# Performance work log

Measured on AMD Instinct MI355X. Metric: run time of the kernel, lower is better.

## Reference

```python
import jax, jax.numpy as jnp
import numpy as np

CIN = 256
WINDOWS = (2, 4, 6)
LN_EPS = 1e-5


def _conv1x1(x, w, b):
    # x: (N,C,H,W), w: (O,C), b: (O,)
    return jnp.einsum('nchw,oc->nohw', x, w) + b[None, :, None, None]


def _pos_encoding(C, H, W):
    # Faithful to SinCosPositionalEncoding2D (incl. its w-major flatten + raw view)
    gw, gh = jnp.meshgrid(jnp.arange(W, dtype=jnp.float32),
                          jnp.arange(H, dtype=jnp.float32), indexing='ij')
    pd = C // 4
    omega = 1.0 / (10000.0 ** (jnp.arange(pd, dtype=jnp.float32) / pd))
    ow = gw.reshape(-1)[:, None] * omega[None, :]
    oh = gh.reshape(-1)[:, None] * omega[None, :]
    pe = jnp.concatenate([jnp.sin(ow), jnp.cos(ow), jnp.sin(oh), jnp.cos(oh)], axis=1)  # (W*H, C)
    return pe.reshape(1, C, H, W)  # raw row-major reinterpret, matching torch .view


def _unfold(x, kh, kw, sh, sw):
    # torch F.unfold semantics: (N,C,H,W) -> (N, C*kh*kw, L), L row-major over (oh, ow)
    N, C, H, W = x.shape
    oh = (H - kh) // sh + 1
    ow = (W - kw) // sw + 1
    ih = (jnp.arange(oh) * sh)[:, None] + jnp.arange(kh)[None, :]  # (oh,kh)
    iw = (jnp.arange(ow) * sw)[:, None] + jnp.arange(kw)[None, :]  # (ow,kw)
    p = x[:, :, ih[:, None, :, None], iw[None, :, None, :]]       # (N,C,oh,ow,kh,kw)
    return jnp.transpose(p, (0, 1, 4, 5, 2, 3)).reshape(N, C * kh * kw, oh * ow)


def _fold(p, H, W, kh, kw, sh, sw):
    # torch F.fold semantics: overlap-add scatter back to (N,C,H,W)
    N = p.shape[0]
    C = p.shape[1] // (kh * kw)
    oh = (H - kh) // sh + 1
    ow = (W - kw) // sw + 1
    p = jnp.transpose(p.reshape(N, C, kh, kw, oh, ow), (0, 1, 4, 5, 2, 3))  # (N,C,oh,ow,kh,kw)
    ih = (jnp.arange(oh) * sh)[:, None] + jnp.arange(kh)[None, :]
    iw = (jnp.arange(ow) * sw)[:, None] + jnp.arange(kw)[None, :]
    out = jnp.zeros((N, C, H, W), p.dtype)
    return out.at[:, :, ih[:, None, :, None], iw[None, :, None, :]].add(p)


def _psa(x, ch_wv_w, ch_wv_b, ch_wq_w, ch_wq_b, ch_wz_w, ch_wz_b, ln_g, ln_b,
         sp_wv_w, sp_wv_b, sp_wq_w, sp_wq_b):
    # Polarized Self-Attention (parallel), input (N,C,H',W')
    N, C, Hh, Ww = x.shape
    C2 = C // 2
    HW = Hh * Ww
    # channel-only branch
    wv = _conv1x1(x, ch_wv_w, ch_wv_b).reshape(N, C2, HW)
    wq = jax.nn.softmax(_conv1x1(x, ch_wq_w, ch_wq_b).reshape(N, HW), axis=-1)
    z = jnp.einsum('ncl,nl->nc', wv, wq)                       # (N, C2)
    wz = jnp.einsum('nc,oc->no', z, ch_wz_w) + ch_wz_b         # (N, C)
    m = wz.mean(-1, keepdims=True)
    v = ((wz - m) ** 2).mean(-1, keepdims=True)
    ch_w = jax.nn.sigmoid((wz - m) / jnp.sqrt(v + LN_EPS) * ln_g + ln_b)
    out_ch = x * ch_w[:, :, None, None]
    # spatial-only branch
    sv = _conv1x1(x, sp_wv_w, sp_wv_b).reshape(N, C2, HW)
    sq = jax.nn.softmax(_conv1x1(x, sp_wq_w, sp_wq_b).mean(axis=(2, 3)), axis=-1)  # (N,C2)
    sp_w = jax.nn.sigmoid(jnp.einsum('nc,ncl->nl', sq, sv)).reshape(N, 1, Hh, Ww)
    return out_ch + x * sp_w


def _forward(x, w_exp, b_exp, w_res, b_res, w_fus, b_fus,
             ch_wv_w, ch_wv_b, ch_wq_w, ch_wq_b, ch_wz_w, ch_wz_b, ln_g, ln_b,
             sp_wv_w, sp_wv_b, sp_wq_w, sp_wq_b):
    N, C, H, W = x.shape
    expx = _conv1x1(x, w_exp, b_exp)                 # (N, 3C, H, W)
    branches = jnp.split(expx, len(WINDOWS), axis=1)
    pos = _pos_encoding(C, H, W)
    outs = []
    for i, win in enumerate(WINDOWS):
        sh, sw = H // win, W // win
        kh, kw = sh + H % win, sw + W % win
        K = kh * kw
        u = _unfold(branches[i], kh, kw, sh, sw).reshape(N, C, win * win, K)
        pu = _unfold(pos, kh, kw, sh, sw).reshape(1, C, win * win, K)
        a = _psa(u + pu, ch_wv_w, ch_wv_b, ch_wq_w, ch_wq_b, ch_wz_w, ch_wz_b,
                 ln_g, ln_b, sp_wv_w, sp_wv_b, sp_wq_w, sp_wq_b)
        a = a.reshape(N, C * K, win * win)           # raw view, matching torch
        cnt = _fold(jnp.ones_like(a), H, W, kh, kw, sh, sw)
        f = _fold(a, H, W, kh, kw, sh, sw) / cnt
        outs.append(f)
    out = _conv1x1(jnp.concatenate(outs, axis=1) + expx, w_res, b_res) + x
    return _conv1x1(out, w_fus, b_fus)


def setup_inputs() -> dict:
    key = jax.random.key(0)
    ks = jax.random.split(key, 10)
    C, C2 = CIN, CIN // 2
    s = 0.02
    nrm = lambda k, shp: jax.random.normal(k, shp, jnp.float32) * s
    return {
        'x': jax.random.normal(ks[0], (8, C, 64, 64), jnp.float32),
        'w_exp': nrm(ks[1], (3 * C, C)), 'b_exp': jnp.zeros((3 * C,), jnp.float32),
        'w_res': nrm(ks[2], (C, 3 * C)), 'b_res': jnp.zeros((C,), jnp.float32),
        'w_fus': nrm(ks[3], (C, C)), 'b_fus': jnp.zeros((C,), jnp.float32),
        'ch_wv_w': nrm(ks[4], (C2, C)), 'ch_wv_b': jnp.zeros((C2,), jnp.float32),
        'ch_wq_w': nrm(ks[5], (1, C)), 'ch_wq_b': jnp.zeros((1,), jnp.float32),
        'ch_wz_w': nrm(ks[6], (C, C2)), 'ch_wz_b': jnp.zeros((C,), jnp.float32),
        'ln_g': jnp.ones((C,), jnp.float32), 'ln_b': jnp.zeros((C,), jnp.float32),
        'sp_wv_w': nrm(ks[7], (C2, C)), 'sp_wv_b': jnp.zeros((C2,), jnp.float32),
        'sp_wq_w': nrm(ks[8], (C2, C)), 'sp_wq_b': jnp.zeros((C2,), jnp.float32),
    }


def reference(x, w_exp, b_exp, w_res, b_res, w_fus, b_fus,
              ch_wv_w, ch_wv_b, ch_wq_w, ch_wq_b, ch_wz_w, ch_wz_b, ln_g, ln_b,
              sp_wv_w, sp_wv_b, sp_wq_w, sp_wq_b):
    return _forward(x, w_exp, b_exp, w_res, b_res, w_fus, b_fus,
                    ch_wv_w, ch_wv_b, ch_wq_w, ch_wq_b, ch_wz_w, ch_wz_b, ln_g, ln_b,
                    sp_wv_w, sp_wv_b, sp_wq_w, sp_wq_b)
```

## Files before the change

### kernel.cpp

```cpp
#include <hip/hip_runtime.h>
#include <cstddef>


#define HW 4096
typedef unsigned short ushort_t;
typedef __attribute__((ext_vector_type(8))) short bf16x8;
typedef __attribute__((ext_vector_type(4))) float floatx4;

__device__ __forceinline__ ushort_t f2bf(float f) {
    unsigned u = __float_as_uint(f);
    u += 0x7FFF + ((u >> 16) & 1);
    return (ushort_t)(u >> 16);
}

__device__ __forceinline__ int cnt1f(int y, int sh, int kh, int win) {
    int t = y - kh + sh;
    int lo = t > 0 ? t / sh : 0;
    int hi = min(win - 1, y / sh);
    return hi - lo + 1;
}

__device__ __forceinline__ float posval(int f) {
    int row = f >> 8, col = f & 255;
    int a = row >> 6, b = row & 63;
    int g = col >> 6, k = col & 63;
    float omega = expf(-(float)k * (9.2103403719761836f / 64.f));
    float arg = (g < 2 ? (float)a : (float)b) * omega;
    return (g & 1) ? cosf(arg) : sinf(arg);
}

__global__ __launch_bounds__(256) void pos_both(
    float* __restrict__ pos, float* __restrict__ posT)
{
    int idx = blockIdx.x * 256 + threadIdx.x;
    pos[idx] = posval(idx);
    int p = idx >> 8, c = idx & 255;
    posT[idx] = posval(c * 4096 + p);
}

__global__ __launch_bounds__(256) void zero_kernel(float* __restrict__ p, int n) {
    int i = blockIdx.x * 256 + threadIdx.x;
    if (i < n) p[i] = 0.f;
}

__global__ __launch_bounds__(256) void trans_x(
    const float* __restrict__ x, ushort_t* __restrict__ xbT)
{
    __shared__ float L[32][37];
    int n = blockIdx.z;
    int p0 = blockIdx.x * 32, c0 = blockIdx.y * 32;
    int t = threadIdx.x;
    int cc = t >> 3, p4 = (t & 7) * 4;
    const float* src = x + (((size_t)(n * 256 + c0 + cc)) << 12) + p0 + p4;
    float4 v = *(const float4*)src;
    L[cc][p4] = v.x; L[cc][p4 + 1] = v.y; L[cc][p4 + 2] = v.z; L[cc][p4 + 3] = v.w;
    __syncthreads();
    int pp = t >> 3, c4 = (t & 7) * 4;
    unsigned lo = (unsigned)f2bf(L[c4][pp]) | ((unsigned)f2bf(L[c4 + 1][pp]) << 16);
    unsigned hi = (unsigned)f2bf(L[c4 + 2][pp]) | ((unsigned)f2bf(L[c4 + 3][pp]) << 16);
    *(uint2*)&xbT[(((size_t)(n << 12)) + p0 + pp) * 256 + c0 + c4] = make_uint2(lo, hi);
}

__global__ __launch_bounds__(256) void conv_bf16(
    const float* __restrict__ src, ushort_t* __restrict__ dst, int nelem)
{
    int i = blockIdx.x * 256 + threadIdx.x;
    if (i < nelem) dst[i] = f2bf(src[i]);
}

__global__ __launch_bounds__(256) void prep_g(
    const float* __restrict__ W_exp, const float* __restrict__ b_exp,
    const float* __restrict__ wq, const float* __restrict__ wq_b,
    float* __restrict__ g, float* __restrict__ c0out)
{
    int i = blockIdx.x, ks = blockIdx.y, tid = threadIdx.x;
    __shared__ float wql[32];
    __shared__ float red[256];
    if (tid < 32) wql[tid] = wq[ks * 32 + tid];
    __syncthreads();
    const float* Wb = W_exp + ((size_t)(i * 256 + ks * 32)) * 256 + tid;
    float acc = 0.f;
    #pragma unroll 8
    for (int j = 0; j < 32; ++j) acc = fmaf(wql[j], Wb[(size_t)j * 256], acc);
    atomicAdd(&g[i * 256 + tid], acc);
    red[tid] = (tid < 32) ? wql[tid] * b_exp[i * 256 + ks * 32 + tid] : 0.f;
    __syncthreads();
    for (int s = 128; s > 0; s >>= 1) { if (tid < s) red[tid] += red[tid + s]; __syncthreads(); }
    if (tid == 0) atomicAdd(&c0out[i], red[0] + (ks == 0 ? wq_b[0] : 0.f));
}

__global__ __launch_bounds__(256) void prep_wcomb(
    const float* __restrict__ W_fus, const float* __restrict__ W_res,
    const float* __restrict__ b_res, const float* __restrict__ b_fus,
    ushort_t* __restrict__ Wcat, float* __restrict__ biasc)
{
    int o = blockIdx.x, jb = blockIdx.y, tid = threadIdx.x;
    __shared__ float wrow[256];
    __shared__ float red[256];
    wrow[tid] = W_fus[o * 256 + tid];
    __syncthreads();
    int j = jb * 256 + tid;
    float acc = 0.f;
    #pragma unroll 8
    for (int c = 0; c < 256; ++c) acc = fmaf(wrow[c], W_res[(size_t)c * 768 + j], acc);
    Wcat[o * 1024 + 256 + j] = f2bf(acc);
    if (jb == 0) {
        Wcat[o * 1024 + tid] = f2bf(wrow[tid]);
        red[tid] = wrow[tid] * b_res[tid];
        __syncthreads();
        for (int s = 128; s > 0; s >>= 1) { if (tid < s) red[tid] += red[tid + s]; __syncthreads(); }
        if (tid == 0) biasc[o] = red[0] + b_fus[o];
    }
}

__global__ __launch_bounds__(256) void xbar_kernel(
    const float* __restrict__ x, const float* __restrict__ pos,
    float* __restrict__ xbar_all, float* __restrict__ xbar6,
    float* __restrict__ posbar, float* __restrict__ posbar6)
{
    int c = blockIdx.x, n = blockIdx.y, tid = threadIdx.x;
    const float* src = (n < 8) ? x + (((size_t)(n * 256 + c)) << 12)
                               : pos + (((size_t)c) << 12);
    float sa = 0.f, s6 = 0.f;
    #pragma unroll
    for (int k = 0; k < 4; ++k) {
        int f4 = tid + k * 256;
        float4 v = *(const float4*)(src + f4 * 4);
        int p = f4 * 4;
        int y = p >> 6, xx = p & 63;
        float cy = (float)cnt1f(y, 10, 14, 6);
        float c0_ = cy * (float)cnt1f(xx + 0, 10, 14, 6);
        float c1_ = cy * (float)cnt1f(xx + 1, 10, 14, 6);
        float c2_ = cy * (float)cnt1f(xx + 2, 10, 14, 6);
        float c3_ = cy * (float)cnt1f(xx + 3, 10, 14, 6);
        sa += v.x + v.y + v.z + v.w;
        s6 += c0_ * v.x + c1_ * v.y + c2_ * v.z + c3_ * v.w;
    }
    __shared__ float red[256];
    red[tid] = sa; __syncthreads();
    for (int s = 128; s > 0; s >>= 1) { if (tid < s) red[tid] += red[tid + s]; __syncthreads(); }
    float ra = red[0]; __syncthreads();
    red[tid] = s6; __syncthreads();
    for (int s = 128; s > 0; s >>= 1) { if (tid < s) red[tid] += red[tid + s]; __syncthreads(); }
    float r6 = red[0];
    if (tid == 0) {
        if (n < 8) { xbar_all[n * 256 + c] = ra; xbar6[n * 256 + c] = r6; }
        else       { posbar[c] = ra;             posbar6[c] = r6; }
    }
}

__global__ __launch_bounds__(512) void qdot_kernel(
    const float* __restrict__ x, const float* __restrict__ pos,
    const float* __restrict__ g, const float* __restrict__ c0in,
    const float* __restrict__ wq, float* __restrict__ qdot)
{
    int n = blockIdx.y, tid = threadIdx.x;
    int ph = tid & 127, cq = tid >> 7;
    int p = blockIdx.x * 128 + ph;
    __shared__ float gl[768];
    __shared__ float wql[256];
    __shared__ float4 red4[512];
    for (int k = tid; k < 768; k += 512) gl[k] = g[k];
    if (tid < 256) wql[tid] = wq[tid];
    __syncthreads();
    const float* xp = x + (((size_t)n) << 20) + p;
    const float* pp = pos + p;
    float q0 = 0.f, q1 = 0.f, q2 = 0.f, qp = 0.f;
    #pragma unroll 4
    for (int c = cq * 64; c < cq * 64 + 64; ++c) {
        float xv = xp[(size_t)c << 12];
        float pv = pp[(size_t)c << 12];
        q0 = fmaf(gl[c], xv, q0);
        q1 = fmaf(gl[256 + c], xv, q1);
        q2 = fmaf(gl[512 + c], xv, q2);
        qp = fmaf(wql[c], pv, qp);
    }
    red4[tid] = make_float4(q0, q1, q2, qp);
    __syncthreads();
    if (tid < 128) {
        float4 a = red4[tid], b = red4[128 + tid], cc = red4[256 + tid], d = red4[384 + tid];
        float rp = a.w + b.w + cc.w + d.w;
        qdot[((0 * 8 + n) << 12) + p] = a.x + b.x + cc.x + d.x + rp + c0in[0];
        qdot[((1 * 8 + n) << 12) + p] = a.y + b.y + cc.y + d.y + rp + c0in[1];
        qdot[((2 * 8 + n) << 12) + p] = a.z + b.z + cc.z + d.z + rp + c0in[2];
    }
}

__global__ __launch_bounds__(256) void ubar_split(
    const float* __restrict__ W_exp, const float* __restrict__ b_exp,
    const float* __restrict__ xbar_all, const float* __restrict__ xbar6,
    const float* __restrict__ posbar, const float* __restrict__ posbar6,
    float* __restrict__ ubar)
{
    int i = blockIdx.x, n = blockIdx.y, ks = blockIdx.z, tid = threadIdx.x;
    int b = i * 8 + n;
    __shared__ float xbl[32];
    const float* xsrc = ((i < 2) ? xbar_all : xbar6) + n * 256 + ks * 32;
    if (tid < 32) xbl[tid] = xsrc[tid];
    __syncthreads();
    const float* Wr = W_exp + ((size_t)(i * 256 + tid)) * 256 + ks * 32;
    float acc = 0.f;
    #pragma unroll 8
    for (int j = 0; j < 32; ++j) acc = fmaf(Wr[j], xbl[j], acc);
    if (ks == 0) {
        int win = 2 * (i + 1), sh = 64 / win, kh = sh + 64 % win;
        float Li = (float)(win * win * kh * kh);
        acc += b_exp[i * 256 + tid] * Li + ((i < 2) ? posbar : posbar6)[tid];
    }
    atomicAdd(&ubar[b * 256 + tid], acc);
}

__global__ __launch_bounds__(256) void pass_b_h(
    const float* __restrict__ qdot, const float* __restrict__ ubar_raw,
    const float* __restrict__ sp_wq_w, const float* __restrict__ sp_wq_b,
    const float* __restrict__ sp_wv_w, const float* __restrict__ sp_wv_b,
    const float* __restrict__ W_exp, const float* __restrict__ b_exp,
    float* __restrict__ Mn, float* __restrict__ invZn,
    float* __restrict__ w_eff, float* __restrict__ h, float* __restrict__ btot)
{
    int i = blockIdx.x, n = blockIdx.y, tid = threadIdx.x;
    int b = i * 8 + n;
    int win = 2 * (i + 1), sh = 64 / win, kh = sh + 64 % win;
    float invL = 1.f / (float)(win * win * kh * kh);
    const float* qd = qdot + (((size_t)b) << 12);
    __shared__ float red[256];
    __shared__ float ub[256];
    __shared__ float spq[128];
    __shared__ float we[256];
    float m = -1e30f;
    for (int p = tid; p < HW; p += 256) m = fmaxf(m, qd[p]);
    red[tid] = m; __syncthreads();
    for (int s = 128; s > 0; s >>= 1) { if (tid < s) red[tid] = fmaxf(red[tid], red[tid + s]); __syncthreads(); }
    float M = red[0]; __syncthreads();
    float z = 0.f;
    for (int p = tid; p < HW; p += 256) {
        int y = p >> 6, xx = p & 63;
        float cf = (float)(cnt1f(y, sh, kh, win) * cnt1f(xx, sh, kh, win));
        z += cf * expf(qd[p] - M);
    }
    red[tid] = z; __syncthreads();
    for (int s = 128; s > 0; s >>= 1) { if (tid < s) red[tid] += red[tid + s]; __syncthreads(); }
    float Z = red[0]; __syncthreads();
    if (tid == 0) { Mn[b] = M; invZn[b] = 1.f / Z; }
    ub[tid] = ubar_raw[b * 256 + tid] * invL;
    __syncthreads();
    float sl = -1e30f;
    if (tid < 128) {
        float a = sp_wq_b[tid];
        #pragma unroll 8
        for (int c = 0; c < 256; ++c) a = fmaf(sp_wq_w[tid * 256 + c], ub[c], a);
        sl = a;
    }
    red[tid] = sl; __syncthreads();
    for (int s = 128; s > 0; s >>= 1) { if (tid < s) red[tid] = fmaxf(red[tid], red[tid + s]); __syncthreads(); }
    float m2 = red[0]; __syncthreads();
    float e = (tid < 128) ? expf(sl - m2) : 0.f;
    red[tid] = e; __syncthreads();
    for (int s = 128; s > 0; s >>= 1) { if (tid < s) red[tid] += red[tid + s]; __syncthreads(); }
    float S2 = red[0]; __syncthreads();
    if (tid < 128) spq[tid] = e / S2;
    __syncthreads();
    float a = 0.f;
    #pragma unroll 8
    for (int c2 = 0; c2 < 128; ++c2) a = fmaf(spq[c2], sp_wv_w[c2 * 256 + tid], a);
    w_eff[b * 256 + tid] = a;
    we[tid] = a;
    red[tid] = (tid < 128) ? spq[tid] * sp_wv_b[tid] : 0.f;
    __syncthreads();
    for (int s = 128; s > 0; s >>= 1) { if (tid < s) red[tid] += red[tid + s]; __syncthreads(); }
    float beff = red[0]; __syncthreads();
    const float* Wb = W_exp + (size_t)i * 65536 + tid;
    float hacc = 0.f;
    #pragma unroll 8
    for (int oc = 0; oc < 256; ++oc) hacc = fmaf(we[oc], Wb[(size_t)oc * 256], hacc);
    h[b * 256 + tid] = hacc;
    red[tid] = we[tid] * b_exp[i * 256 + tid];
    __syncthreads();
    for (int s = 128; s > 0; s >>= 1) { if (tid < s) red[tid] += red[tid + s]; __syncthreads(); }
    if (tid == 0) btot[b] = red[0] + beff;
}

__global__ __launch_bounds__(512) void spw_t_kernel(
    const float* __restrict__ x, const float* __restrict__ pos,
    const float* __restrict__ h, const float* __restrict__ weff,
    const float* __restrict__ qdot, const float* __restrict__ Mn,
    const float* __restrict__ invZn, const float* __restrict__ btot,
    float* __restrict__ spw, float* __restrict__ tbuf)
{
    int n = blockIdx.y, tid = threadIdx.x;
    int ph = tid & 127, cq = tid >> 7;
    int p = blockIdx.x * 128 + ph;
    __shared__ float hl[768], wl[768];
    __shared__ float4 red4[512];
    for (int k = tid; k < 768; k += 512) {
        int i = k >> 8, c = k & 255;
        hl[k] = h[(i * 8 + n) * 256 + c];
        wl[k] = weff[(i * 8 + n) * 256 + c];
    }
    __syncthreads();
    const float* xp = x + (((size_t)n) << 20) + p;
    const float* pp = pos + p;
    float a0 = 0.f, a1 = 0.f, a2 = 0.f;
    #pragma unroll 4
    for (int c = cq * 64; c < cq * 64 + 64; ++c) {
        float xv = xp[(size_t)c << 12];
        float pv = pp[(size_t)c << 12];
        a0 += hl[c] * xv + wl[c] * pv;
        a1 += hl[256 + c] * xv + wl[256 + c] * pv;
        a2 += hl[512 + c] * xv + wl[512 + c] * pv;
    }
    red4[tid] = make_float4(a0, a1, a2, 0.f);
    __syncthreads();
    if (tid < 128) {
        float4 aa = red4[tid], bb = red4[128 + tid], cc = red4[256 + tid], dd = red4[384 + tid];
        float av[3] = {aa.x + bb.x + cc.x + dd.x,
                       aa.y + bb.y + cc.y + dd.y,
                       aa.z + bb.z + cc.z + dd.z};
        int y = p >> 6, xx = p & 63;
        #pragma unroll
        for (int i = 0; i < 3; ++i) {
            int b = i * 8 + n;
            int win = 2 * (i + 1), sh = 64 / win, kh = sh + 64 % win;
            float cf = (float)(cnt1f(y, sh, kh, win) * cnt1f(xx, sh, kh, win));
            int idx = (b << 12) + p;
            spw[idx] = 1.f / (1.f + expf(-(av[i] + btot[b])));
            tbuf[idx] = cf * expf(qdot[idx] - Mn[b]) * invZn[b];
        }
    }
}

__global__ __launch_bounds__(256) void xq_kernel(
    const float* __restrict__ x, const float* __restrict__ pos,
    const float* __restrict__ tbuf, float* __restrict__ xq, float* __restrict__ posq)
{
    int c = blockIdx.x, n = blockIdx.y, tid = threadIdx.x;
    const float* xr = x + (((size_t)(n * 256 + c)) << 12);
    const float* pr = pos + (((size_t)c) << 12);
    float ax[3] = {0.f, 0.f, 0.f}, ap[3] = {0.f, 0.f, 0.f};
    #pragma unroll
    for (int k = 0; k < 4; ++k) {
        int f4 = tid + k * 256;
        float4 xv = *(const float4*)(xr + f4 * 4);
        float4 pv = *(const float4*)(pr + f4 * 4);
        #pragma unroll
        for (int i = 0; i < 3; ++i) {
            float4 tv = *(const float4*)(tbuf + (((size_t)(i * 8 + n)) << 12) + f4 * 4);
            ax[i] += tv.x * xv.x + tv.y * xv.y + tv.z * xv.z + tv.w * xv.w;
            ap[i] += tv.x * pv.x + tv.y * pv.y + tv.z * pv.z + tv.w * pv.w;
        }
    }
    __shared__ float red[256];
    #pragma unroll
    for (int i = 0; i < 3; ++i) {
        red[tid] = ax[i]; __syncthreads();
        for (int s = 128; s > 0; s >>= 1) { if (tid < s) red[tid] += red[tid + s]; __syncthreads(); }
        float rx = red[0]; __syncthreads();
        red[tid] = ap[i]; __syncthreads();
        for (int s = 128; s > 0; s >>= 1) { if (tid < s) red[tid] += red[tid + s]; __syncthreads(); }
        float rp = red[0]; __syncthreads();
        if (tid == 0) { xq[(i * 8 + n) * 256 + c] = rx; posq[(i * 8 + n) * 256 + c] = rp; }
    }
}

__global__ __launch_bounds__(256) void pass_d_uq(
    const float* __restrict__ W_exp, const float* __restrict__ b_exp,
    const float* __restrict__ xq, const float* __restrict__ posq,
    const float* __restrict__ ch_wv_w, const float* __restrict__ ch_wv_b,
    const float* __restrict__ ch_wz_w, const float* __restrict__ ch_wz_b,
    const float* __restrict__ ln_g, const float* __restrict__ ln_b,
    float* __restrict__ ch_w)
{
    int i = blockIdx.x, n = blockIdx.y, tid = threadIdx.x;
    int b = i * 8 + n;
    __shared__ float xql[256];
    __shared__ float uql[256];
    __shared__ float zz[128];
    __shared__ float red[256];
    xql[tid] = xq[b * 256 + tid];
    __syncthreads();
    float acc = b_exp[i * 256 + tid] + posq[b * 256 + tid];
    const float* Wr = W_exp + ((size_t)(i * 256 + tid)) * 256;
    #pragma unroll 8
    for (int cin = 0; cin < 256; ++cin) acc = fmaf(Wr[cin], xql[cin], acc);
    uql[tid] = acc;
    __syncthreads();
    if (tid < 128) {
        float a = ch_wv_b[tid];
        #pragma unroll 8
        for (int c = 0; c < 256; ++c) a = fmaf(ch_wv_w[tid * 256 + c], uql[c], a);
        zz[tid] = a;
    }
    __syncthreads();
    float wz = ch_wz_b[tid];
    #pragma unroll 8
    for (int c2 = 0; c2 < 128; ++c2) wz = fmaf(ch_wz_w[tid * 128 + c2], zz[c2], wz);
    red[tid] = wz; __syncthreads();
    for (int s = 128; s > 0; s >>= 1) { if (tid < s) red[tid] += red[tid + s]; __syncthreads(); }
    float mean = red[0] * (1.f / 256.f); __syncthreads();
    float d = wz - mean;
    red[tid] = d * d; __syncthreads();
    for (int s = 128; s > 0; s >>= 1) { if (tid < s) red[tid] += red[tid + s]; __syncthreads(); }
    float var = red[0] * (1.f / 256.f);
    float xn = d / sqrtf(var + 1e-5f);
    ch_w[b * 256 + tid] = 1.f / (1.f + expf(-(xn * ln_g[tid] + ln_b[tid])));
}

__global__ __launch_bounds__(256) void gemm_expT(
    const ushort_t* __restrict__ Wb, const ushort_t* __restrict__ XT,
    const float* __restrict__ bias, const float* __restrict__ posT,
    const float* __restrict__ chw, const float* __restrict__ spw,
    ushort_t* __restrict__ OutT)
{
    __shared__ ushort_t As[128 * 40];
    __shared__ ushort_t Bs[128 * 40];
    int n = blockIdx.z;
    int p0 = blockIdx.x * 128;
    int o0 = blockIdx.y * 128;
    int t = threadIdx.x;
    int lane = t & 63, wave = t >> 6;
    int wm = (wave & 1) * 64, wn = (wave >> 1) * 64;
    int lr = lane & 15, lk = (lane >> 4) * 8;
    int ar = t >> 2, ac = (t & 3) * 8;
    const ushort_t* A0 = Wb + (size_t)(o0 + ar) * 256 + ac;
    const ushort_t* A1 = Wb + (size_t)(o0 + ar + 64) * 256 + ac;
    const ushort_t* B0 = XT + (((size_t)(n << 12)) + p0 + ar) * 256 + ac;
    const ushort_t* B1 = XT + (((size_t)(n << 12)) + p0 + ar + 64) * 256 + ac;
    floatx4 acc[4][4] = {};
    for (int k0 = 0; k0 < 256; k0 += 32) {
        uint4 a0 = *(const uint4*)(A0 + k0);
        uint4 a1 = *(const uint4*)(A1 + k0);
        uint4 b0 = *(const uint4*)(B0 + k0);
        uint4 b1 = *(const uint4*)(B1 + k0);
        __syncthreads();
        *(uint4*)&As[ar * 40 + ac] = a0;
        *(uint4*)&As[(ar + 64) * 40 + ac] = a1;
        *(uint4*)&Bs[ar * 40 + ac] = b0;
        *(uint4*)&Bs[(ar + 64) * 40 + ac] = b1;
        __syncthreads();
        bf16x8 af[4], bfr[4];
        #pragma unroll
        for (int mi = 0; mi < 4; ++mi)
            af[mi] = *(const bf16x8*)&As[(wm + mi * 16 + lr) * 40 + lk];
        #pragma unroll
        for (int ni = 0; ni < 4; ++ni)
            bfr[ni] = *(const bf16x8*)&Bs[(wn + ni * 16 + lr) * 40 + lk];
        #pragma unroll
        for (int mi = 0; mi < 4; ++mi)
            #pragma unroll
            for (int ni = 0; ni < 4; ++ni)
                acc[mi][ni] = __builtin_amdgcn_mfma_f32_16x16x32_bf16(
                    af[mi], bfr[ni], acc[mi][ni], 0, 0, 0);
    }
    int col = lane & 15, rb = (lane >> 4) * 4;
    int ibr = o0 >> 8;
    int bi = ibr * 8 + n;
    float sv[4]; int pv_[4];
    #pragma unroll
    for (int ni = 0; ni < 4; ++ni) {
        int p = p0 + wn + ni * 16 + col;
        pv_[ni] = p;
        sv[ni] = spw[(bi << 12) + p];
    }
    #pragma unroll
    for (int mi = 0; mi < 4; ++mi) {
        int o = o0 + wm + mi * 16 + rb;
        int c = o & 255;
        float4 bo = *(const float4*)&bias[o];
        float4 cw = *(const float4*)&chw[bi * 256 + c];
        #pragma unroll
        for (int ni = 0; ni < 4; ++ni) {
            int p = pv_[ni];
            float4 q = *(const float4*)&posT[p * 256 + c];
            floatx4 v = acc[mi][ni];
            float s = sv[ni];
            float e0 = v[0] + bo.x, e1 = v[1] + bo.y, e2 = v[2] + bo.z, e3 = v[3] + bo.w;
            float r0 = e0 + (e0 + q.x) * (cw.x + s);
            float r1 = e1 + (e1 + q.y) * (cw.y + s);
            float r2 = e2 + (e2 + q.z) * (cw.z + s);
            float r3 = e3 + (e3 + q.w) * (cw.w + s);
            unsigned lo = (unsigned)f2bf(r0) | ((unsigned)f2bf(r1) << 16);
            unsigned hi = (unsigned)f2bf(r2) | ((unsigned)f2bf(r3) << 16);
            *(uint2*)&OutT[(((size_t)(n << 12)) + p) * 768 + o] = make_uint2(lo, hi);
        }
    }
}

__global__ __launch_bounds__(256) void gemm_out(
    const ushort_t* __restrict__ Wcat, const ushort_t* __restrict__ XT,
    const ushort_t* __restrict__ CT, const float* __restrict__ biasc,
    float* __restrict__ Out)
{
    __shared__ ushort_t As[128 * 40];
    __shared__ ushort_t Bs[128 * 40];
    int n = blockIdx.z;
    int p0 = blockIdx.x * 128;
    int o0 = blockIdx.y * 128;
    int t = threadIdx.x;
    int lane = t & 63, wave = t >> 6;
    int wm = (wave & 1) * 64, wn = (wave >> 1) * 64;
    int lr = lane & 15, lk = (lane >> 4) * 8;
    int ar = t >> 2, ac = (t & 3) * 8;
    const ushort_t* A0 = Wcat + (size_t)(o0 + ar) * 1024 + ac;
    const ushort_t* A1 = Wcat + (size_t)(o0 + ar + 64) * 1024 + ac;
    const ushort_t* BX0 = XT + (((size_t)(n << 12)) + p0 + ar) * 256 + ac;
    const ushort_t* BX1 = XT + (((size_t)(n << 12)) + p0 + ar + 64) * 256 + ac;
    const ushort_t* BC0 = CT + (((size_t)(n << 12)) + p0 + ar) * 768 + ac;
    const ushort_t* BC1 = CT + (((size_t)(n << 12)) + p0 + ar + 64) * 768 + ac;
    floatx4 acc[4][4] = {};
    for (int k0 = 0; k0 < 1024; k0 += 32) {
        const ushort_t* pb0 = (k0 < 256) ? (BX0 + k0) : (BC0 + (k0 - 256));
        const ushort_t* pb1 = (k0 < 256) ? (BX1 + k0) : (BC1 + (k0 - 256));
        uint4 a0 = *(const uint4*)(A0 + k0);
        uint4 a1 = *(const uint4*)(A1 + k0);
        uint4 b0 = *(const uint4*)pb0;
        uint4 b1 = *(const uint4*)pb1;
        __syncthreads();
        *(uint4*)&As[ar * 40 + ac] = a0;
        *(uint4*)&As[(ar + 64) * 40 + ac] = a1;
        *(uint4*)&Bs[ar * 40 + ac] = b0;
        *(uint4*)&Bs[(ar + 64) * 40 + ac] = b1;
        __syncthreads();
        bf16x8 af[4], bfr[4];
        #pragma unroll
        for (int mi = 0; mi < 4; ++mi)
            af[mi] = *(const bf16x8*)&As[(wm + mi * 16 + lr) * 40 + lk];
        #pragma unroll
        for (int ni = 0; ni < 4; ++ni)
            bfr[ni] = *(const bf16x8*)&Bs[(wn + ni * 16 + lr) * 40 + lk];
        #pragma unroll
        for (int mi = 0; mi < 4; ++mi)
            #pragma unroll
            for (int ni = 0; ni < 4; ++ni)
                acc[mi][ni] = __builtin_amdgcn_mfma_f32_16x16x32_bf16(
                    af[mi], bfr[ni], acc[mi][ni], 0, 0, 0);
    }
    int col = lane & 15, rb = (lane >> 4) * 4;
    #pragma unroll
    for (int mi = 0; mi < 4; ++mi) {
        int o = o0 + wm + mi * 16 + rb;
        float4 bo = *(const float4*)&biasc[o];
        #pragma unroll
        for (int r = 0; r < 4; ++r) {
            float br = (r == 0) ? bo.x : (r == 1) ? bo.y : (r == 2) ? bo.z : bo.w;
            #pragma unroll
            for (int ni = 0; ni < 4; ++ni) {
                int p = p0 + wn + ni * 16 + col;
                Out[(((size_t)(n * 256 + o + r)) << 12) + p] = acc[mi][ni][r] + br;
            }
        }
    }
}

extern "C" void kernel_launch(void* const* d_in, const int* in_sizes, int n_in,
                              void* d_out, int out_size, void* d_ws, size_t ws_size,
                              hipStream_t stream) {
    const float* x        = (const float*)d_in[0];
    const float* w_exp    = (const float*)d_in[1];
    const float* b_exp    = (const float*)d_in[2];
    const float* w_res    = (const float*)d_in[3];
    const float* b_res    = (const float*)d_in[4];
    const float* w_fus    = (const float*)d_in[5];
    const float* b_fus    = (const float*)d_in[6];
    const float* ch_wv_w  = (const float*)d_in[7];
    const float* ch_wv_b  = (const float*)d_in[8];
    const float* ch_wq_w  = (const float*)d_in[9];
    const float* ch_wq_b  = (const float*)d_in[10];
    const float* ch_wz_w  = (const float*)d_in[11];
    const float* ch_wz_b  = (const float*)d_in[12];
    const float* ln_g     = (const float*)d_in[13];
    const float* ln_b     = (const float*)d_in[14];
    const float* sp_wv_w  = (const float*)d_in[15];
    const float* sp_wv_b  = (const float*)d_in[16];
    const float* sp_wq_w  = (const float*)d_in[17];
    const float* sp_wq_b  = (const float*)d_in[18];
    float* out = (float*)d_out;
    float* ws  = (float*)d_ws;

    float*    pos   = ws + 0;
    float*    posT  = ws + 1048576;
    ushort_t* xbT   = (ushort_t*)(ws + 2097152);
    ushort_t* exT   = (ushort_t*)(ws + 6291456);
    ushort_t* wexpb = (ushort_t*)(ws + 18874368);
    ushort_t* Wcat  = (ushort_t*)(ws + 18972672);
    float*    qdot  = ws + 19103744;
    float*    tbuf  = ws + 19202048;
    float*    spw   = ws + 19300352;
    float*    g     = ws + 19398656;
    float*    c0v   = ws + 19399424;
    float*    ubar  = ws + 19399428;
    float*    xba   = ws + 19405572;
    float*    xb6   = ws + 19407620;
    float*    pba   = ws + 19409668;
    float*    pb6   = ws + 19409924;
    float*    Mn    = ws + 19410180;
    float*    iZ    = ws + 19410204;
    float*    weff  = ws + 19410228;
    float*    btot  = ws + 19416372;
    float*    hb    = ws + 19416396;
    float*    xq    = ws + 19422540;
    float*    posq  = ws + 19428684;
    float*    chw   = ws + 19434828;
    float*    biasc = ws + 19440972;

    pos_both<<<4096, 256, 0, stream>>>(pos, posT);
    zero_kernel<<<28, 256, 0, stream>>>(g, 6916);
    trans_x<<<dim3(128, 8, 8), 256, 0, stream>>>(x, xbT);
    conv_bf16<<<768, 256, 0, stream>>>(w_exp, wexpb, 196608);
    prep_g<<<dim3(3, 8), 256, 0, stream>>>(w_exp, b_exp, ch_wq_w, ch_wq_b, g, c0v);
    prep_wcomb<<<dim3(256, 3), 256, 0, stream>>>(w_fus, w_res, b_res, b_fus, Wcat, biasc);

    xbar_kernel<<<dim3(256, 9), 256, 0, stream>>>(x, pos, xba, xb6, pba, pb6);
    qdot_kernel<<<dim3(32, 8), 512, 0, stream>>>(x, pos, g, c0v, ch_wq_w, qdot);
    ubar_split<<<dim3(3, 8, 8), 256, 0, stream>>>(w_exp, b_exp, xba, xb6, pba, pb6, ubar);
    pass_b_h<<<dim3(3, 8), 256, 0, stream>>>(qdot, ubar, sp_wq_w, sp_wq_b,
                                             sp_wv_w, sp_wv_b, w_exp, b_exp,
                                             Mn, iZ, weff, hb, btot);
    spw_t_kernel<<<dim3(32, 8), 512, 0, stream>>>(x, pos, hb, weff, qdot, Mn, iZ,
                                                  btot, spw, tbuf);
    xq_kernel<<<dim3(256, 8), 256, 0, stream>>>(x, pos, tbuf, xq, posq);
    pass_d_uq<<<dim3(3, 8), 256, 0, stream>>>(w_exp, b_exp, xq, posq,
                                              ch_wv_w, ch_wv_b, ch_wz_w, ch_wz_b,
                                              ln_g, ln_b, chw);

    gemm_expT<<<dim3(32, 6, 8), 256, 0, stream>>>(wexpb, xbT, b_exp, posT, chw, spw, exT);
    gemm_out<<<dim3(32, 2, 8), 256, 0, stream>>>(Wcat, xbT, exT, biasc, out);
}
```

Baseline: 309.0 us.

## Merge prep kernels, fuse qdot/ubar and spw/xq, stage gemm_expT epilogue via LDS

The six setup kernels become one block-indexed prep_all launch, and qdot and ubar share a single launch. The tbuf intermediate is removed: spw_t_xq computes the softmax weights into LDS and reduces them against bf16 xbT and posT with atomics into xq/posq. The gemm_expT epilogue now stages the accumulators through LDS so posT/chw loads and output stores become wide, coalesced row writes. The goal is fewer launches and less global traffic, at the cost of atomics, bf16 rounding of x in xq, and an extra bf16 round trip of the GEMM result before the epilogue.

After: 291.4 us. 5.7% less time.

```diff
diff --git a/kernel.cpp b/kernel.cpp
--- a/kernel.cpp
+++ b/kernel.cpp
@@ -11,6 +11,9 @@
     unsigned u = __float_as_uint(f);
     u += 0x7FFF + ((u >> 16) & 1);
     return (ushort_t)(u >> 16);
+}
+__device__ __forceinline__ float bf2f(ushort_t h) {
+    return __uint_as_float(((unsigned)h) << 16);
 }
 
 __device__ __forceinline__ int cnt1f(int y, int sh, int kh, int win) {
@@ -29,87 +32,77 @@
     return (g & 1) ? cosf(arg) : sinf(arg);
 }
 
-__global__ __launch_bounds__(256) void pos_both(
-    float* __restrict__ pos, float* __restrict__ posT)
-{
-    int idx = blockIdx.x * 256 + threadIdx.x;
-    pos[idx] = posval(idx);
-    int p = idx >> 8, c = idx & 255;
-    posT[idx] = posval(c * 4096 + p);
-}
-
-__global__ __launch_bounds__(256) void zero_kernel(float* __restrict__ p, int n) {
-    int i = blockIdx.x * 256 + threadIdx.x;
-    if (i < n) p[i] = 0.f;
-}
-
-__global__ __launch_bounds__(256) void trans_x(
-    const float* __restrict__ x, ushort_t* __restrict__ xbT)
-{
-    __shared__ float L[32][37];
-    int n = blockIdx.z;
-    int p0 = blockIdx.x * 32, c0 = blockIdx.y * 32;
-    int t = threadIdx.x;
-    int cc = t >> 3, p4 = (t & 7) * 4;
-    const float* src = x + (((size_t)(n * 256 + c0 + cc)) << 12) + p0 + p4;
-    float4 v = *(const float4*)src;
-    L[cc][p4] = v.x; L[cc][p4 + 1] = v.y; L[cc][p4 + 2] = v.z; L[cc][p4 + 3] = v.w;
-    __syncthreads();
-    int pp = t >> 3, c4 = (t & 7) * 4;
-    unsigned lo = (unsigned)f2bf(L[c4][pp]) | ((unsigned)f2bf(L[c4 + 1][pp]) << 16);
-    unsigned hi = (unsigned)f2bf(L[c4 + 2][pp]) | ((unsigned)f2bf(L[c4 + 3][pp]) << 16);
-    *(uint2*)&xbT[(((size_t)(n << 12)) + p0 + pp) * 256 + c0 + c4] = make_uint2(lo, hi);
-}
-
-__global__ __launch_bounds__(256) void conv_bf16(
-    const float* __restrict__ src, ushort_t* __restrict__ dst, int nelem)
-{
-    int i = blockIdx.x * 256 + threadIdx.x;
-    if (i < nelem) dst[i] = f2bf(src[i]);
-}
-
-__global__ __launch_bounds__(256) void prep_g(
-    const float* __restrict__ W_exp, const float* __restrict__ b_exp,
-    const float* __restrict__ wq, const float* __restrict__ wq_b,
-    float* __restrict__ g, float* __restrict__ c0out)
-{
-    int i = blockIdx.x, ks = blockIdx.y, tid = threadIdx.x;
-    __shared__ float wql[32];
-    __shared__ float red[256];
-    if (tid < 32) wql[tid] = wq[ks * 32 + tid];
-    __syncthreads();
-    const float* Wb = W_exp + ((size_t)(i * 256 + ks * 32)) * 256 + tid;
-    float acc = 0.f;
-    #pragma unroll 8
-    for (int j = 0; j < 32; ++j) acc = fmaf(wql[j], Wb[(size_t)j * 256], acc);
-    atomicAdd(&g[i * 256 + tid], acc);
-    red[tid] = (tid < 32) ? wql[tid] * b_exp[i * 256 + ks * 32 + tid] : 0.f;
-    __syncthreads();
-    for (int s = 128; s > 0; s >>= 1) { if (tid < s) red[tid] += red[tid + s]; __syncthreads(); }
-    if (tid == 0) atomicAdd(&c0out[i], red[0] + (ks == 0 ? wq_b[0] : 0.f));
-}
-
-__global__ __launch_bounds__(256) void prep_wcomb(
-    const float* __restrict__ W_fus, const float* __restrict__ W_res,
-    const float* __restrict__ b_res, const float* __restrict__ b_fus,
-    ushort_t* __restrict__ Wcat, float* __restrict__ biasc)
-{
-    int o = blockIdx.x, jb = blockIdx.y, tid = threadIdx.x;
-    __shared__ float wrow[256];
-    __shared__ float red[256];
-    wrow[tid] = W_fus[o * 256 + tid];
-    __syncthreads();
-    int j = jb * 256 + tid;
-    float acc = 0.f;
-    #pragma unroll 8
-    for (int c = 0; c < 256; ++c) acc = fmaf(wrow[c], W_res[(size_t)c * 768 + j], acc);
-    Wcat[o * 1024 + 256 + j] = f2bf(acc);
-    if (jb == 0) {
-        Wcat[o * 1024 + tid] = f2bf(wrow[tid]);
-        red[tid] = wrow[tid] * b_res[tid];
-        __syncthreads();
+__global__ __launch_bounds__(256) void prep_all(
+    const float* __restrict__ x, const float* __restrict__ W_exp,
+    const float* __restrict__ b_exp, const float* __restrict__ wq,
+    const float* __restrict__ wq_b, const float* __restrict__ W_fus,
+    const float* __restrict__ W_res, const float* __restrict__ b_res,
+    const float* __restrict__ b_fus,
+    float* __restrict__ pos, float* __restrict__ posT,
+    ushort_t* __restrict__ xbT, ushort_t* __restrict__ wexpb,
+    float* __restrict__ g, float* __restrict__ c0out,
+    ushort_t* __restrict__ Wcat, float* __restrict__ biasc,
+    float* __restrict__ zeroreg)
+{
+    __shared__ float smf[1184];
+    int b = blockIdx.x, tid = threadIdx.x;
+    if (b < 4096) {
+        int idx = b * 256 + tid;
+        pos[idx] = posval(idx);
+        int p = idx >> 8, c = idx & 255;
+        posT[idx] = posval(c * 4096 + p);
+    } else if (b < 12288) {
+        int v = b - 4096;
+        int p0 = (v & 127) * 32, c0 = ((v >> 7) & 7) * 32, n = v >> 10;
+        int cc = tid >> 3, p4 = (tid & 7) * 4;
+        const float* src = x + (((size_t)(n * 256 + c0 + cc)) << 12) + p0 + p4;
+        float4 vv = *(const float4*)src;
+        smf[cc * 37 + p4] = vv.x; smf[cc * 37 + p4 + 1] = vv.y;
+        smf[cc * 37 + p4 + 2] = vv.z; smf[cc * 37 + p4 + 3] = vv.w;
+        __syncthreads();
+        int pp = tid >> 3, c4 = (tid & 7) * 4;
+        unsigned lo = (unsigned)f2bf(smf[c4 * 37 + pp]) | ((unsigned)f2bf(smf[(c4 + 1) * 37 + pp]) << 16);
+        unsigned hi = (unsigned)f2bf(smf[(c4 + 2) * 37 + pp]) | ((unsigned)f2bf(smf[(c4 + 3) * 37 + pp]) << 16);
+        *(uint2*)&xbT[(((size_t)(n << 12)) + p0 + pp) * 256 + c0 + c4] = make_uint2(lo, hi);
+    } else if (b < 13056) {
+        int i = (b - 12288) * 256 + tid;
+        wexpb[i] = f2bf(W_exp[i]);
+    } else if (b < 13059) {
+        int i = b - 13056;
+        float* wql = smf;
+        float* red = smf + 256;
+        wql[tid] = wq[tid];
+        red[tid] = wq[tid] * b_exp[i * 256 + tid];
+        __syncthreads();
+        const float* Wb = W_exp + ((size_t)(i * 256)) * 256 + tid;
+        float acc = 0.f;
+        #pragma unroll 8
+        for (int oc = 0; oc < 256; ++oc) acc = fmaf(wql[oc], Wb[(size_t)oc * 256], acc);
+        g[i * 256 + tid] = acc;
         for (int s = 128; s > 0; s >>= 1) { if (tid < s) red[tid] += red[tid + s]; __syncthreads(); }
-        if (tid == 0) biasc[o] = red[0] + b_fus[o];
+        if (tid == 0) c0out[i] = red[0] + wq_b[0];
+    } else if (b < 13827) {
+        int v = b - 13059;
+        int o = v & 255, jb = v >> 8;
+        float* wrow = smf;
+        float* red = smf + 256;
+        wrow[tid] = W_fus[o * 256 + tid];
+        __syncthreads();
+        int j = jb * 256 + tid;
+        float acc = 0.f;
+        #pragma unroll 8
+        for (int c = 0; c < 256; ++c) acc = fmaf(wrow[c], W_res[(size_t)c * 768 + j], acc);
+        Wcat[o * 1024 + 256 + j] = f2bf(acc);
+        if (jb == 0) {
+            Wcat[o * 1024 + tid] = f2bf(wrow[tid]);
+            red[tid] = wrow[tid] * b_res[tid];
+            __syncthreads();
+            for (int s = 128; s > 0; s >>= 1) { if (tid < s) red[tid] += red[tid + s]; __syncthreads(); }
+            if (tid == 0) biasc[o] = red[0] + b_fus[o];
+        }
+    } else {
+        int i = (b - 13827) * 256 + tid;
+        zeroreg[i] = 0.f;
     }
 }
 
@@ -149,65 +142,63 @@
     }
 }
 
-__global__ __launch_bounds__(512) void qdot_kernel(
+__global__ __launch_bounds__(512) void qdot_ubar(
     const float* __restrict__ x, const float* __restrict__ pos,
     const float* __restrict__ g, const float* __restrict__ c0in,
-    const float* __restrict__ wq, float* __restrict__ qdot)
-{
-    int n = blockIdx.y, tid = threadIdx.x;
-    int ph = tid & 127, cq = tid >> 7;
-    int p = blockIdx.x * 128 + ph;
-    __shared__ float gl[768];
-    __shared__ float wql[256];
-    __shared__ float4 red4[512];
-    for (int k = tid; k < 768; k += 512) gl[k] = g[k];
-    if (tid < 256) wql[tid] = wq[tid];
-    __syncthreads();
-    const float* xp = x + (((size_t)n) << 20) + p;
-    const float* pp = pos + p;
-    float q0 = 0.f, q1 = 0.f, q2 = 0.f, qp = 0.f;
-    #pragma unroll 4
-    for (int c = cq * 64; c < cq * 64 + 64; ++c) {
-        float xv = xp[(size_t)c << 12];
-        float pv = pp[(size_t)c << 12];
-        q0 = fmaf(gl[c], xv, q0);
-        q1 = fmaf(gl[256 + c], xv, q1);
-        q2 = fmaf(gl[512 + c], xv, q2);
-        qp = fmaf(wql[c], pv, qp);
-    }
-    red4[tid] = make_float4(q0, q1, q2, qp);
-    __syncthreads();
-    if (tid < 128) {
-        float4 a = red4[tid], b = red4[128 + tid], cc = red4[256 + tid], d = red4[384 + tid];
-        float rp = a.w + b.w + cc.w + d.w;
-        qdot[((0 * 8 + n) << 12) + p] = a.x + b.x + cc.x + d.x + rp + c0in[0];
-        qdot[((1 * 8 + n) << 12) + p] = a.y + b.y + cc.y + d.y + rp + c0in[1];
-        qdot[((2 * 8 + n) << 12) + p] = a.z + b.z + cc.z + d.z + rp + c0in[2];
-    }
-}
-
-__global__ __launch_bounds__(256) void ubar_split(
+    const float* __restrict__ wq, float* __restrict__ qdot,
     const float* __restrict__ W_exp, const float* __restrict__ b_exp,
     const float* __restrict__ xbar_all, const float* __restrict__ xbar6,
     const float* __restrict__ posbar, const float* __restrict__ posbar6,
     float* __restrict__ ubar)
 {
-    int i = blockIdx.x, n = blockIdx.y, ks = blockIdx.z, tid = threadIdx.x;
-    int b = i * 8 + n;
-    __shared__ float xbl[32];
-    const float* xsrc = ((i < 2) ? xbar_all : xbar6) + n * 256 + ks * 32;
-    if (tid < 32) xbl[tid] = xsrc[tid];
-    __syncthreads();
-    const float* Wr = W_exp + ((size_t)(i * 256 + tid)) * 256 + ks * 32;
-    float acc = 0.f;
-    #pragma unroll 8
-    for (int j = 0; j < 32; ++j) acc = fmaf(Wr[j], xbl[j], acc);
-    if (ks == 0) {
-        int win = 2 * (i + 1), sh = 64 / win, kh = sh + 64 % win;
-        float Li = (float)(win * win * kh * kh);
-        acc += b_exp[i * 256 + tid] * Li + ((i < 2) ? posbar : posbar6)[tid];
-    }
-    atomicAdd(&ubar[b * 256 + tid], acc);
+    int blk = blockIdx.x, tid = threadIdx.x;
+    if (blk < 256) {
+        int n = blk >> 5;
+        int ph = tid & 127, cq = tid >> 7;
+        int p = (blk & 31) * 128 + ph;
+        __shared__ float gl[768];
+        __shared__ float wql[256];
+        __shared__ float4 red4[512];
+        for (int k = tid; k < 768; k += 512) gl[k] = g[k];
+        if (tid < 256) wql[tid] = wq[tid];
+        __syncthreads();
+        const float* xp = x + (((size_t)n) << 20) + p;
+        const float* pp = pos + p;
+        float q0 = 0.f, q1 = 0.f, q2 = 0.f, qp = 0.f;
+        #pragma unroll 4
+        for (int c = cq * 64; c < cq * 64 + 64; ++c) {
+            float xv = xp[(size_t)c << 12];
+            float pv = pp[(size_t)c << 12];
+            q0 = fmaf(gl[c], xv, q0);
+            q1 = fmaf(gl[256 + c], xv, q1);
+            q2 = fmaf(gl[512 + c], xv, q2);
+            qp = fmaf(wql[c], pv, qp);
+        }
+        red4[tid] = make_float4(q0, q1, q2, qp);
+        __syncthreads();
+        if (tid < 128) {
+            float4 a = red4[tid], b = red4[128 + tid], cc = red4[256 + tid], d = red4[384 + tid];
+            float rp = a.w + b.w + cc.w + d.w;
+            qdot[((0 * 8 + n) << 12) + p] = a.x + b.x + cc.x + d.x + rp + c0in[0];
+            qdot[((1 * 8 + n) << 12) + p] = a.y + b.y + cc.y + d.y + rp + c0in[1];
+            qdot[((2 * 8 + n) << 12) + p] = a.z + b.z + cc.z + d.z + rp + c0in[2];
+        }
+    } else {
+        int v = blk - 256;
+        int i = v >> 3, n = v & 7;
+        __shared__ float xbl[256];
+        if (tid < 256) xbl[tid] = ((i < 2) ? xbar_all : xbar6)[n * 256 + tid];
+        __syncthreads();
+        if (tid < 256) {
+            int win = 2 * (i + 1), sh = 64 / win, kh = sh + 64 % win;
+            float Li = (float)(win * win * kh * kh);
+            float acc = b_exp[i * 256 + tid] * Li + ((i < 2) ? posbar : posbar6)[tid];
+            const float* Wr = W_exp + ((size_t)(i * 256 + tid)) * 256;
+            #pragma unroll 8
+            for (int j = 0; j < 256; ++j) acc = fmaf(Wr[j], xbl[j], acc);
+            ubar[(i * 8 + n) * 256 + tid] = acc;
+        }
+    }
 }
 
 __global__ __launch_bounds__(256) void pass_b_h(
@@ -280,18 +271,21 @@
     if (tid == 0) btot[b] = red[0] + beff;
 }
 
-__global__ __launch_bounds__(512) void spw_t_kernel(
+__global__ __launch_bounds__(512) void spw_t_xq(
     const float* __restrict__ x, const float* __restrict__ pos,
     const float* __restrict__ h, const float* __restrict__ weff,
     const float* __restrict__ qdot, const float* __restrict__ Mn,
     const float* __restrict__ invZn, const float* __restrict__ btot,
-    float* __restrict__ spw, float* __restrict__ tbuf)
+    const ushort_t* __restrict__ xbT, const float* __restrict__ posT,
+    float* __restrict__ spw, float* __restrict__ xq, float* __restrict__ posq)
 {
     int n = blockIdx.y, tid = threadIdx.x;
     int ph = tid & 127, cq = tid >> 7;
-    int p = blockIdx.x * 128 + ph;
+    int p0b = blockIdx.x * 128;
+    int p = p0b + ph;
     __shared__ float hl[768], wl[768];
     __shared__ float4 red4[512];
+    __shared__ float tl[3][128];
     for (int k = tid; k < 768; k += 512) {
         int i = k >> 8, c = k & 255;
         hl[k] = h[(i * 8 + n) * 256 + c];
@@ -324,41 +318,37 @@
             float cf = (float)(cnt1f(y, sh, kh, win) * cnt1f(xx, sh, kh, win));
             int idx = (b << 12) + p;
             spw[idx] = 1.f / (1.f + expf(-(av[i] + btot[b])));
-            tbuf[idx] = cf * expf(qdot[idx] - Mn[b]) * invZn[b];
-        }
-    }
-}
-
-__global__ __launch_bounds__(256) void xq_kernel(
-    const float* __restrict__ x, const float* __restrict__ pos,
-    const float* __restrict__ tbuf, float* __restrict__ xq, float* __restrict__ posq)
-{
-    int c = blockIdx.x, n = blockIdx.y, tid = threadIdx.x;
-    const float* xr = x + (((size_t)(n * 256 + c)) << 12);
-    const float* pr = pos + (((size_t)c) << 12);
-    float ax[3] = {0.f, 0.f, 0.f}, ap[3] = {0.f, 0.f, 0.f};
-    #pragma unroll
-    for (int k = 0; k < 4; ++k) {
-        int f4 = tid + k * 256;
-        float4 xv = *(const float4*)(xr + f4 * 4);
-        float4 pv = *(const float4*)(pr + f4 * 4);
-        #pragma unroll
-        for (int i = 0; i < 3; ++i) {
-            float4 tv = *(const float4*)(tbuf + (((size_t)(i * 8 + n)) << 12) + f4 * 4);
-            ax[i] += tv.x * xv.x + tv.y * xv.y + tv.z * xv.z + tv.w * xv.w;
-            ap[i] += tv.x * pv.x + tv.y * pv.y + tv.z * pv.z + tv.w * pv.w;
-        }
-    }
-    __shared__ float red[256];
-    #pragma unroll
-    for (int i = 0; i < 3; ++i) {
-        red[tid] = ax[i]; __syncthreads();
-        for (int s = 128; s > 0; s >>= 1) { if (tid < s) red[tid] += red[tid + s]; __syncthreads(); }
-        float rx = red[0]; __syncthreads();
-        red[tid] = ap[i]; __syncthreads();
-        for (int s = 128; s > 0; s >>= 1) { if (tid < s) red[tid] += red[tid + s]; __syncthreads(); }
-        float rp = red[0]; __syncthreads();
-        if (tid == 0) { xq[(i * 8 + n) * 256 + c] = rx; posq[(i * 8 + n) * 256 + c] = rp; }
+            tl[i][ph] = cf * expf(qdot[idx] - Mn[b]) * invZn[b];
+        }
+    }
+    __syncthreads();
+    int c = tid & 255;
+    int half = tid >> 8;
+    float s0 = 0.f, s1 = 0.f, s2 = 0.f;
+    if (half == 0) {
+        const ushort_t* xb = xbT + (((size_t)((n << 12) + p0b)) << 8) + c;
+        #pragma unroll 4
+        for (int pl = 0; pl < 128; ++pl) {
+            float xv = bf2f(xb[(size_t)pl << 8]);
+            s0 = fmaf(tl[0][pl], xv, s0);
+            s1 = fmaf(tl[1][pl], xv, s1);
+            s2 = fmaf(tl[2][pl], xv, s2);
+        }
+        atomicAdd(&xq[(0 * 8 + n) * 256 + c], s0);
+        atomicAdd(&xq[(1 * 8 + n) * 256 + c], s1);
+        atomicAdd(&xq[(2 * 8 + n) * 256 + c], s2);
+    } else {
+        const float* pt = posT + (((size_t)p0b) << 8) + c;
+        #pragma unroll 4
+        for (int pl = 0; pl < 128; ++pl) {
+            float pv = pt[(size_t)pl << 8];
+            s0 = fmaf(tl[0][pl], pv, s0);
+            s1 = fmaf(tl[1][pl], pv, s1);
+            s2 = fmaf(tl[2][pl], pv, s2);
+        }
+        atomicAdd(&posq[(0 * 8 + n) * 256 + c], s0);
+        atomicAdd(&posq[(1 * 8 + n) * 256 + c], s1);
+        atomicAdd(&posq[(2 * 8 + n) * 256 + c], s2);
     }
 }
 
@@ -411,8 +401,9 @@
     const float* __restrict__ chw, const float* __restrict__ spw,
     ushort_t* __restrict__ OutT)
 {
-    __shared__ ushort_t As[128 * 40];
-    __shared__ ushort_t Bs[128 * 40];
+    __shared__ ushort_t SM[10240];
+    ushort_t* As = SM;
+    ushort_t* Bs = SM + 5120;
     int n = blockIdx.z;
     int p0 = blockIdx.x * 128;
     int o0 = blockIdx.y * 128;
@@ -454,33 +445,55 @@
     int col = lane & 15, rb = (lane >> 4) * 4;
     int ibr = o0 >> 8;
     int bi = ibr * 8 + n;
-    float sv[4]; int pv_[4];
     #pragma unroll
-    for (int ni = 0; ni < 4; ++ni) {
-        int p = p0 + wn + ni * 16 + col;
-        pv_[ni] = p;
-        sv[ni] = spw[(bi << 12) + p];
-    }
-    #pragma unroll
-    for (int mi = 0; mi < 4; ++mi) {
-        int o = o0 + wm + mi * 16 + rb;
-        int c = o & 255;
-        float4 bo = *(const float4*)&bias[o];
-        float4 cw = *(const float4*)&chw[bi * 256 + c];
-        #pragma unroll
-        for (int ni = 0; ni < 4; ++ni) {
-            int p = pv_[ni];
-            float4 q = *(const float4*)&posT[p * 256 + c];
-            floatx4 v = acc[mi][ni];
-            float s = sv[ni];
-            float e0 = v[0] + bo.x, e1 = v[1] + bo.y, e2 = v[2] + bo.z, e3 = v[3] + bo.w;
-            float r0 = e0 + (e0 + q.x) * (cw.x + s);
-            float r1 = e1 + (e1 + q.y) * (cw.y + s);
-            float r2 = e2 + (e2 + q.z) * (cw.z + s);
-            float r3 = e3 + (e3 + q.w) * (cw.w + s);
-            unsigned lo = (unsigned)f2bf(r0) | ((unsigned)f2bf(r1) << 16);
-            unsigned hi = (unsigned)f2bf(r2) | ((unsigned)f2bf(r3) << 16);
-            *(uint2*)&OutT[(((size_t)(n << 12)) + p) * 768 + o] = make_uint2(lo, hi);
+    for (int r = 0; r < 2; ++r) {
+        __syncthreads();
+        if (wm == r * 64) {
+            #pragma unroll
+            for (int mi = 0; mi < 4; ++mi) {
+                int o_loc = mi * 16 + rb;
+                float4 bo = *(const float4*)&bias[o0 + r * 64 + o_loc];
+                #pragma unroll
+                for (int ni = 0; ni < 4; ++ni) {
+                    int prow = wn + ni * 16 + col;
+                    floatx4 v = acc[mi][ni];
+                    unsigned lo = (unsigned)f2bf(v[0] + bo.x) | ((unsigned)f2bf(v[1] + bo.y) << 16);
+                    unsigned hi = (unsigned)f2bf(v[2] + bo.z) | ((unsigned)f2bf(v[3] + bo.w) << 16);
+                    *(uint2*)&SM[prow * 72 + o_loc] = make_uint2(lo, hi);
+                }
+            }
+        }
+        __syncthreads();
+        #pragma unroll
+        for (int it = 0; it < 4; ++it) {
+            int slot = it * 256 + t;
+            int pl = slot >> 3, j = (slot & 7) * 8;
+            uint4 raw = *(const uint4*)&SM[pl * 72 + j];
+            float e0 = bf2f((ushort_t)(raw.x & 0xFFFF)), e1 = bf2f((ushort_t)(raw.x >> 16));
+            float e2 = bf2f((ushort_t)(raw.y & 0xFFFF)), e3 = bf2f((ushort_t)(raw.y >> 16));
+            float e4 = bf2f((ushort_t)(raw.z & 0xFFFF)), e5 = bf2f((ushort_t)(raw.z >> 16));
+            float e6 = bf2f((ushort_t)(raw.w & 0xFFFF)), e7 = bf2f((ushort_t)(raw.w >> 16));
+            int p = p0 + pl;
+            int cbase = (o0 & 255) + r * 64 + j;
+            float s = spw[(bi << 12) + p];
+            float4 q0 = *(const float4*)&posT[p * 256 + cbase];
+            float4 q1 = *(const float4*)&posT[p * 256 + cbase + 4];
+            float4 w0 = *(const float4*)&chw[bi * 256 + cbase];
+            float4 w1 = *(const float4*)&chw[bi * 256 + cbase + 4];
+            float r0 = e0 + (e0 + q0.x) * (w0.x + s);
+            float r1 = e1 + (e1 + q0.y) * (w0.y + s);
+            float r2 = e2 + (e2 + q0.z) * (w0.z + s);
+            float r3 = e3 + (e3 + q0.w) * (w0.w + s);
+            float r4 = e4 + (e4 + q1.x) * (w1.x + s);
+            float r5 = e5 + (e5 + q1.y) * (w1.y + s);
+            float r6 = e6 + (e6 + q1.z) * (w1.z + s);
+            float r7 = e7 + (e7 + q1.w) * (w1.w + s);
+            uint4 outv;
+            outv.x = (unsigned)f2bf(r0) | ((unsigned)f2bf(r1) << 16);
+            outv.y = (unsigned)f2bf(r2) | ((unsigned)f2bf(r3) << 16);
+            outv.z = (unsigned)f2bf(r4) | ((unsigned)f2bf(r5) << 16);
+            outv.w = (unsigned)f2bf(r6) | ((unsigned)f2bf(r7) << 16);
+            *(uint4*)&OutT[(((size_t)(n << 12)) + p) * 768 + o0 + r * 64 + j] = outv;
         }
     }
 }
@@ -583,7 +596,6 @@
     ushort_t* wexpb = (ushort_t*)(ws + 18874368);
     ushort_t* Wcat  = (ushort_t*)(ws + 18972672);
     float*    qdot  = ws + 19103744;
-    float*    tbuf  = ws + 19202048;
     float*    spw   = ws + 19300352;
     float*    g     = ws + 19398656;
     float*    c0v   = ws + 19399424;
@@ -602,26 +614,21 @@
     float*    chw   = ws + 19434828;
     float*    biasc = ws + 19440972;
 
-    pos_both<<<4096, 256, 0, stream>>>(pos, posT);
-    zero_kernel<<<28, 256, 0, stream>>>(g, 6916);
-    trans_x<<<dim3(128, 8, 8), 256, 0, stream>>>(x, xbT);
-    conv_bf16<<<768, 256, 0, stream>>>(w_exp, wexpb, 196608);
-    prep_g<<<dim3(3, 8), 256, 0, stream>>>(w_exp, b_exp, ch_wq_w, ch_wq_b, g, c0v);
-    prep_wcomb<<<dim3(256, 3), 256, 0, stream>>>(w_fus, w_res, b_res, b_fus, Wcat, biasc);
-
+    prep_all<<<13875, 256, 0, stream>>>(x, w_exp, b_exp, ch_wq_w, ch_wq_b,
+                                        w_fus, w_res, b_res, b_fus,
+                                        pos, posT, xbT, wexpb, g, c0v,
+                                        Wcat, biasc, xq);
     xbar_kernel<<<dim3(256, 9), 256, 0, stream>>>(x, pos, xba, xb6, pba, pb6);
-    qdot_kernel<<<dim3(32, 8), 512, 0, stream>>>(x, pos, g, c0v, ch_wq_w, qdot);
-    ubar_split<<<dim3(3, 8, 8), 256, 0, stream>>>(w_exp, b_exp, xba, xb6, pba, pb6, ubar);
+    qdot_ubar<<<280, 512, 0, stream>>>(x, pos, g, c0v, ch_wq_w, qdot,
+                                       w_exp, b_exp, xba, xb6, pba, pb6, ubar);
     pass_b_h<<<dim3(3, 8), 256, 0, stream>>>(qdot, ubar, sp_wq_w, sp_wq_b,
                                              sp_wv_w, sp_wv_b, w_exp, b_exp,
                                              Mn, iZ, weff, hb, btot);
-    spw_t_kernel<<<dim3(32, 8), 512, 0, stream>>>(x, pos, hb, weff, qdot, Mn, iZ,
-                                                  btot, spw, tbuf);
-    xq_kernel<<<dim3(256, 8), 256, 0, stream>>>(x, pos, tbuf, xq, posq);
+    spw_t_xq<<<dim3(32, 8), 512, 0, stream>>>(x, pos, hb, weff, qdot, Mn, iZ,
+                                              btot, xbT, posT, spw, xq, posq);
     pass_d_uq<<<dim3(3, 8), 256, 0, stream>>>(w_exp, b_exp, xq, posq,
                                               ch_wv_w, ch_wv_b, ch_wz_w, ch_wz_b,
                                               ln_g, ln_b, chw);
-
     gemm_expT<<<dim3(32, 6, 8), 256, 0, stream>>>(wexpb, xbT, b_exp, posT, chw, spw, exT);
     gemm_out<<<dim3(32, 2, 8), 256, 0, stream>>>(Wcat, xbT, exT, biasc, out);
 }
```
